# Optimization experiments

Measured on AMD Instinct MI355X. Metric: run time of the kernel, lower is better.

## Reference

```python
import jax, jax.numpy as jnp
import numpy as np


def _mlp2(x, W1, b1, W2, b2):
    # Linear -> (BN=identity in eval) -> ReLU -> Linear  (on_last=False: no act on last)
    return jax.nn.relu(x @ W1 + b1) @ W2 + b2


def _layer(x, ef, row, col, pos, p):
    N, Dn = x.shape
    E, De = ef.shape
    (qW, qB, kW, kB, vW, vB, dW1, dB1, dW2, dB2, eW1, eB1, eW2, eB2,
     attW1, attB1, attW2, attB2, nW1, nB1, nW2, nB2, aW, aB) = p
    d_ep = attW2.shape[0]
    H = De // d_ep
    temp = jnp.sqrt(jnp.asarray(d_ep, x.dtype))
    # ---- reverse-edge lookup: for edge (i,j), find edge (j,i) if present ----
    keys = row.astype(jnp.int64) * N + col.astype(jnp.int64)
    rkeys = col.astype(jnp.int64) * N + row.astype(jnp.int64)
    order = jnp.argsort(keys)
    sk = keys[order]
    loc = jnp.clip(jnp.searchsorted(sk, rkeys), 0, E - 1)
    found = sk[loc] == rkeys
    rev = jnp.where(found[:, None], ef[order[loc]], 0.0)  # [E, De]
    # ---- distance mask ----
    diff = pos[row] - pos[col]                              # [E,3]
    dist = jnp.linalg.norm(diff, axis=1, keepdims=True)     # [E,1]
    dfeat = jnp.concatenate([diff, dist], axis=1)           # [E,4]
    dm = jax.nn.sigmoid(_mlp2(dfeat, dW1, dB1, dW2, dB2))[:, 0]  # [E]
    # ---- message ----
    x_i = x[row]
    x_j = x[col]
    upd_edge = _mlp2(jnp.concatenate([x_i, ef, rev, x_j], axis=1), eW1, eB1, eW2, eB2)  # [E,De]
    q = (x_i @ qW + qB).reshape(E, Dn // H, H)              # [E, d_np, H]
    k = (ef @ kW + kB).reshape(E, d_ep, H)                  # [E, d_ep, H]
    v = x_j @ vW + vB                                       # [E, Da]
    h = jnp.concatenate([q, k], axis=1)                     # [E, d_np+d_ep, H]
    h1 = jax.nn.relu(jnp.einsum('ech,oc->eoh', h, attW1) + attB1[None, :, None])
    att = jnp.einsum('ech,oc->eoh', h1, attW2) + attB2[None, :, None]  # [E, d_ep, H]
    att = att * dm[:, None, None]
    prob = jax.nn.softmax(att / temp, axis=1)               # softmax over channel dim
    wv = prob.reshape(E, -1) * v                            # [E, Da]
    # ---- aggregate (scatter max over source node) ----
    agg = jax.ops.segment_max(wv, row, num_segments=N)
    agg = jnp.where(jnp.isneginf(agg), 0.0, agg)
    # ---- node update ----
    upd_node = _mlp2(jnp.concatenate([x, agg], axis=1), nW1, nB1, nW2, nB2)  # [N,Dn]
    # ---- twin-edge attention (mean of updated edges over out/in edges) ----
    ones = jnp.ones((E,), x.dtype)
    dout = jnp.maximum(jax.ops.segment_sum(ones, row, num_segments=N), 1.0)
    din = jnp.maximum(jax.ops.segment_sum(ones, col, num_segments=N), 1.0)
    outf = jax.ops.segment_sum(upd_edge, row, num_segments=N) / dout[:, None]
    incf = jax.ops.segment_sum(upd_edge, col, num_segments=N) / din[:, None]
    eatt = jax.nn.sigmoid(jnp.concatenate([outf, incf], axis=1) @ aW + aB)  # [N,De]
    final = jax.nn.relu(upd_node) * eatt
    return final, upd_edge, prob


def setup_inputs() -> dict:
    N, E, Dn, De, Da, H, L = 10000, 160000, 128, 128, 128, 8, 2
    d_np, d_ep = Dn // H, De // H
    rng = np.random.default_rng(0)
    half = E // 2
    r = rng.integers(0, N, half)
    c = rng.integers(0, N, half)
    edges = jnp.asarray(np.stack([np.concatenate([r, c]), np.concatenate([c, r])]), dtype=jnp.int32)
    ks = iter(jax.random.split(jax.random.key(0), 40))
    def p(*shape, s=0.02):
        return jax.random.normal(next(ks), shape, jnp.float32) * s
    return dict(
        node_feature=p(N, Dn, s=1.0),
        edge_feature=p(E, De, s=1.0),
        edges_indices=edges,
        descriptor=p(N, 8, s=1.0),
        qW=p(L, Dn, Dn), qB=p(L, Dn),
        kW=p(L, De, De), kB=p(L, De),
        vW=p(L, Dn, Da), vB=p(L, Da),
        dW1=p(L, 4, 32), dB1=p(L, 32),
        dW2=p(L, 32, 1), dB2=p(L, 1),
        eW1=p(L, 2 * Dn + 2 * De, Dn + 2 * De), eB1=p(L, Dn + 2 * De),
        eW2=p(L, Dn + 2 * De, De), eB2=p(L, De),
        attW1=p(L, d_np + d_ep, d_np + d_ep), attB1=p(L, d_np + d_ep),
        attW2=p(L, d_ep, d_np + d_ep), attB2=p(L, d_ep),
        nW1=p(L, Dn + Da, Dn + De), nB1=p(L, Dn + De),
        nW2=p(L, Dn + De, Dn), nB2=p(L, Dn),
        aW=p(L, 2 * De, De), aB=p(L, De),
    )


def reference(node_feature, edge_feature, edges_indices, descriptor,
              qW, qB, kW, kB, vW, vB, dW1, dB1, dW2, dB2,
              eW1, eB1, eW2, eB2, attW1, attB1, attW2, attB2,
              nW1, nB1, nW2, nB2, aW, aB):
    row, col = edges_indices[0], edges_indices[1]
    pos = descriptor[:, :3]
    L = qW.shape[0]
    x, ef = node_feature, edge_feature
    probs = []
    for l in range(L):
        p = (qW[l], qB[l], kW[l], kB[l], vW[l], vB[l], dW1[l], dB1[l], dW2[l], dB2[l],
             eW1[l], eB1[l], eW2[l], eB2[l], attW1[l], attB1[l], attW2[l], attB2[l],
             nW1[l], nB1[l], nW2[l], nB2[l], aW[l], aB[l])
        x, ef, prob = _layer(x, ef, row, col, pos, p)
        if l < L - 1 or L == 1:
            x = jax.nn.relu(x)
            ef = jax.nn.relu(ef)
        probs.append(prob)
    return x, ef, jnp.stack(probs)
```

## Files before the change

kernel.cpp:

```cpp
#include <hip/hip_runtime.h>
#include <math.h>

#define HS 524288
#define HSM (HS - 1)
#define ENC_NEGINF 0x007FFFFFu

__device__ __forceinline__ unsigned encf(float f) {
    unsigned b = __float_as_uint(f);
    return (b & 0x80000000u) ? ~b : (b | 0x80000000u);
}
__device__ __forceinline__ float decf(unsigned u) {
    return __uint_as_float((u & 0x80000000u) ? (u & 0x7FFFFFFFu) : ~u);
}

__device__ __forceinline__ unsigned short f2bf(float x) {
    unsigned u = __float_as_uint(x);
    unsigned r = u + 0x7FFFu + ((u >> 16) & 1u);
    return (unsigned short)(r >> 16);
}
__device__ __forceinline__ float bf2f(unsigned short h) {
    return __uint_as_float(((unsigned)h) << 16);
}

using bfrag = __attribute__((ext_vector_type(8))) short;
using ffrag = __attribute__((ext_vector_type(4))) float;

__device__ __forceinline__ void split8(const float* f, bfrag& hi, bfrag& lo) {
#pragma unroll
    for (int j = 0; j < 8; ++j) {
        unsigned short h = f2bf(f[j]);
        hi[j] = (short)h;
        lo[j] = (short)f2bf(f[j] - bf2f(h));
    }
}


__global__ __launch_bounds__(256) void k_init_static(unsigned* hashK, int* hashV,
                                                     int* rowcnt, int* colcnt, int N) {
    int i = blockIdx.x * 256 + threadIdx.x;
    if (i < HS) { hashK[i] = 0xFFFFFFFFu; hashV[i] = 0x7FFFFFFF; }
    if (i < N) { rowcnt[i] = 0; colcnt[i] = 0; }
}

__global__ __launch_bounds__(256) void k_hash_insert(const int* __restrict__ row,
                                                     const int* __restrict__ col,
                                                     unsigned* hashK, int* hashV, int N, int E) {
    int e = blockIdx.x * 256 + threadIdx.x;
    if (e >= E) return;
    unsigned key = (unsigned)row[e] * (unsigned)N + (unsigned)col[e];
    unsigned h = (key * 2654435761u) >> 13; h &= HSM;
    while (true) {
        unsigned prev = atomicCAS(&hashK[h], 0xFFFFFFFFu, key);
        if (prev == 0xFFFFFFFFu || prev == key) { atomicMin(&hashV[h], e); break; }
        h = (h + 1) & HSM;
    }
}

__global__ __launch_bounds__(256) void k_hash_lookup(const int* __restrict__ row,
                                                     const int* __restrict__ col,
                                                     const unsigned* __restrict__ hashK,
                                                     const int* __restrict__ hashV,
                                                     int* __restrict__ ridx,
                                                     int* rowcnt, int* colcnt, int N, int E) {
    int e = blockIdx.x * 256 + threadIdx.x;
    if (e >= E) return;
    int r = row[e], c = col[e];
    unsigned rkey = (unsigned)c * (unsigned)N + (unsigned)r;
    unsigned h = (rkey * 2654435761u) >> 13; h &= HSM;
    int res = -1;
    while (true) {
        unsigned kk = hashK[h];
        if (kk == rkey) { res = hashV[h]; break; }
        if (kk == 0xFFFFFFFFu) break;
        h = (h + 1) & HSM;
    }
    ridx[e] = res;
    atomicAdd(&rowcnt[r], 1);
    atomicAdd(&colcnt[c], 1);
}

__global__ __launch_bounds__(256) void k_layer_init(unsigned* aggenc, float* outf, float* incf, int NC) {
    int i = blockIdx.x * 256 + threadIdx.x;
    if (i >= NC) return;
    aggenc[i] = ENC_NEGINF;
    outf[i] = 0.f;
    incf[i] = 0.f;
}

__global__ __launch_bounds__(256) void k_prep_wt(const float* __restrict__ src,
                                                 unsigned short* __restrict__ whi,
                                                 unsigned short* __restrict__ wlo,
                                                 int K, int Nn) {
    int idx = blockIdx.x * 256 + threadIdx.x;
    if (idx >= K * Nn) return;
    int k = idx / Nn, n = idx - k * Nn;
    float v = src[idx];
    unsigned short h = f2bf(v);
    float hf = bf2f(h);
    unsigned short l = f2bf(v - hf);
    whi[(size_t)n * K + k] = h;
    wlo[(size_t)n * K + k] = l;
}

template <int ACT>
__global__ __launch_bounds__(256) void k_gemm(const float* __restrict__ A,
                                              const float* __restrict__ B,
                                              const float* __restrict__ bias,
                                              float* __restrict__ C,
                                              int M, int Nd, int K, int lda, int ldb, int ldc) {
    __shared__ float As[16][64];
    __shared__ float Bs[16][64];
    const int tid = threadIdx.x;
    const int bm = blockIdx.y * 64, bn = blockIdx.x * 64;
    const int tx = tid & 15, ty = tid >> 4;
    const int mload = tid >> 2, k4 = (tid & 3) << 2;
    const int kload = tid >> 4, n4 = (tid & 15) << 2;
    float acc[4][4] = {};
    const int gmload = bm + mload;
    const bool avalid = (gmload < M);
    const float* aptr = A + (size_t)(avalid ? gmload : (M - 1)) * lda + k4;
    const float* bptr = B + (size_t)kload * ldb + bn + n4;
    for (int kb = 0; kb < K; kb += 16) {
        float4 av = avalid ? *(const float4*)(aptr + kb) : make_float4(0.f, 0.f, 0.f, 0.f);
        As[k4 + 0][mload] = av.x; As[k4 + 1][mload] = av.y;
        As[k4 + 2][mload] = av.z; As[k4 + 3][mload] = av.w;
        *(float4*)&Bs[kload][n4] = *(const float4*)(bptr + (size_t)kb * ldb);
        __syncthreads();
#pragma unroll
        for (int k = 0; k < 16; ++k) {
            float4 a = *(const float4*)&As[k][ty << 2];
            float4 b = *(const float4*)&Bs[k][tx << 2];
            acc[0][0] += a.x * b.x; acc[0][1] += a.x * b.y; acc[0][2] += a.x * b.z; acc[0][3] += a.x * b.w;
            acc[1][0] += a.y * b.x; acc[1][1] += a.y * b.y; acc[1][2] += a.y * b.z; acc[1][3] += a.y * b.w;
            acc[2][0] += a.z * b.x; acc[2][1] += a.z * b.y; acc[2][2] += a.z * b.z; acc[2][3] += a.z * b.w;
            acc[3][0] += a.w * b.x; acc[3][1] += a.w * b.y; acc[3][2] += a.w * b.z; acc[3][3] += a.w * b.w;
        }
        __syncthreads();
    }
#pragma unroll
    for (int i = 0; i < 4; ++i) {
        int gm = bm + (ty << 2) + i;
        if (gm >= M) continue;
        float* crow = C + (size_t)gm * ldc;
#pragma unroll
        for (int j = 0; j < 4; ++j) {
            int gn = bn + (tx << 2) + j;
            float v = acc[i][j];
            if (bias) v += bias[gn];
            if (ACT == 1) v = fmaxf(v, 0.f);
            if (ACT == 2) v = 1.f / (1.f + __expf(-v));
            crow[gn] = v;
        }
    }
}


#define LDP 40

template <int MODE, int KSTEPS>
__global__ __launch_bounds__(256) void k_mfma_gemm(const float* __restrict__ Asrc,
                                                   const int* __restrict__ ridx,
                                                   const unsigned short* __restrict__ Bhi,
                                                   const unsigned short* __restrict__ Blo,
                                                   const float* __restrict__ bias,
                                                   const float* __restrict__ xa,
                                                   const float* __restrict__ xb,
                                                   const int* __restrict__ rowArr,
                                                   const int* __restrict__ colArr,
                                                   float* __restrict__ outC,
                                                   float* __restrict__ outf,
                                                   float* __restrict__ incf,
                                                   int edgeBase, int Mrows, int reluOut) {
    constexpr int K = KSTEPS * 32;
    __shared__ unsigned short Ah[128 * LDP];
    __shared__ unsigned short Al[128 * LDP];
    __shared__ unsigned short Bh[128 * LDP];
    __shared__ unsigned short Bl[128 * LDP];

    const int tid = threadIdx.x;
    const int bm = blockIdx.y * 128;
    const int bx = blockIdx.x;

    const int sr = tid >> 1;
    const int kh = (tid & 1) * 16;

    const float* p0;
    const float* p1 = nullptr;
    {
        int rc = min(bm + sr, Mrows - 1);
        if (MODE == 0) {
            int e = edgeBase + rc;
            p0 = Asrc + (size_t)e * 128;
            int rv = ridx[e];
            p1 = (rv >= 0) ? (Asrc + (size_t)rv * 128) : nullptr;
        } else if (MODE == 1) {
            p0 = Asrc + (size_t)rc * 384;
        } else {
            p0 = Asrc + (size_t)rc * 128;
        }
    }
    const unsigned short* bhp = Bhi + (size_t)(bx * 128 + sr) * K + kh;
    const unsigned short* blp = Blo + (size_t)(bx * 128 + sr) * K + kh;

    const int wid = tid >> 6;
    const int lane = tid & 63;
    const int wr0 = (wid >> 1) * 64;
    const int wc0 = (wid & 1) * 64;
    const int lm = lane & 15;
    const int lk = (lane >> 4) * 8;

    ffrag acc[4][4];
#pragma unroll
    for (int i = 0; i < 4; ++i)
#pragma unroll
        for (int j = 0; j < 4; ++j)
            acc[i][j] = (ffrag){0.f, 0.f, 0.f, 0.f};

    unsigned short* AhW = &Ah[sr * LDP + kh];
    unsigned short* AlW = &Al[sr * LDP + kh];
    unsigned short* BhW = &Bh[sr * LDP + kh];
    unsigned short* BlW = &Bl[sr * LDP + kh];

    for (int ks = 0; ks < KSTEPS; ++ks) {
        const int kb = ks * 32;
        const float* ap;
        if (MODE == 0) ap = (kb < 128) ? (p0 + kb) : (p1 ? p1 + (kb - 128) : nullptr);
        else ap = p0 + kb;
#pragma unroll
        for (int c = 0; c < 4; ++c) {
            float4 f = ap ? *(const float4*)(ap + kh + c * 4) : make_float4(0.f, 0.f, 0.f, 0.f);
            ushort4 h, l;
            h.x = f2bf(f.x); l.x = f2bf(f.x - bf2f(h.x));
            h.y = f2bf(f.y); l.y = f2bf(f.y - bf2f(h.y));
            h.z = f2bf(f.z); l.z = f2bf(f.z - bf2f(h.z));
            h.w = f2bf(f.w); l.w = f2bf(f.w - bf2f(h.w));
            *(ushort4*)(AhW + c * 4) = h;
            *(ushort4*)(AlW + c * 4) = l;
        }
        {
            uint4 b0 = *(const uint4*)(bhp + kb);
            uint4 b1 = *(const uint4*)(bhp + kb + 8);
            uint4 c0 = *(const uint4*)(blp + kb);
            uint4 c1 = *(const uint4*)(blp + kb + 8);
            *(uint4*)(BhW) = b0; *(uint4*)(BhW + 8) = b1;
            *(uint4*)(BlW) = c0; *(uint4*)(BlW + 8) = c1;
        }
        __syncthreads();
        bfrag a_h[4], a_l[4], b_h[4], b_l[4];
#pragma unroll
        for (int mt = 0; mt < 4; ++mt) {
            int base = (wr0 + mt * 16 + lm) * LDP + lk;
            a_h[mt] = *(const bfrag*)&Ah[base];
            a_l[mt] = *(const bfrag*)&Al[base];
        }
#pragma unroll
        for (int nt = 0; nt < 4; ++nt) {
            int base = (wc0 + nt * 16 + lm) * LDP + lk;
            b_h[nt] = *(const bfrag*)&Bh[base];
            b_l[nt] = *(const bfrag*)&Bl[base];
        }
#pragma unroll
        for (int mt = 0; mt < 4; ++mt)
#pragma unroll
            for (int nt = 0; nt < 4; ++nt) {
                acc[mt][nt] = __builtin_amdgcn_mfma_f32_16x16x32_bf16(a_h[mt], b_h[nt], acc[mt][nt], 0, 0, 0);
                acc[mt][nt] = __builtin_amdgcn_mfma_f32_16x16x32_bf16(a_l[mt], b_h[nt], acc[mt][nt], 0, 0, 0);
                acc[mt][nt] = __builtin_amdgcn_mfma_f32_16x16x32_bf16(a_h[mt], b_l[nt], acc[mt][nt], 0, 0, 0);
            }
        __syncthreads();
    }

    float bv[4];
#pragma unroll
    for (int nt = 0; nt < 4; ++nt) bv[nt] = bias[bx * 128 + wc0 + nt * 16 + lm];

#pragma unroll
    for (int mt = 0; mt < 4; ++mt) {
#pragma unroll
        for (int i = 0; i < 4; ++i) {
            int grow = bm + wr0 + mt * 16 + (lane >> 4) * 4 + i;
            if (grow >= Mrows) continue;
            if (MODE == 0) {
                int e = edgeBase + grow;
                size_t re = (size_t)rowArr[e] * 384;
                size_t ce = (size_t)colArr[e] * 384;
                float* crow = outC + (size_t)grow * 384;
#pragma unroll
                for (int nt = 0; nt < 4; ++nt) {
                    int gcol = bx * 128 + wc0 + nt * 16 + lm;
                    float v = acc[mt][nt][i] + bv[nt] + xa[re + gcol] + xb[ce + gcol];
                    crow[gcol] = fmaxf(v, 0.f);
                }
            } else if (MODE == 1) {
                int e = edgeBase + grow;
                size_t re = (size_t)rowArr[e] * 128;
                size_t ce = (size_t)colArr[e] * 128;
                float* crow = outC + (size_t)e * 128;
#pragma unroll
                for (int nt = 0; nt < 4; ++nt) {
                    int gcol = wc0 + nt * 16 + lm;
                    float v = acc[mt][nt][i] + bv[nt];
                    atomicAdd(&outf[re + gcol], v);
                    atomicAdd(&incf[ce + gcol], v);
                    crow[gcol] = reluOut ? fmaxf(v, 0.f) : v;
                }
            } else {
                float* crow = outC + (size_t)grow * 128;
#pragma unroll
                for (int nt = 0; nt < 4; ++nt) {
                    int gcol = wc0 + nt * 16 + lm;
                    crow[gcol] = acc[mt][nt][i] + bv[nt];
                }
            }
        }
    }
}


__global__ __launch_bounds__(256) void k_dm(const float* __restrict__ desc,
                                            const int* __restrict__ row,
                                            const int* __restrict__ col,
                                            const float* __restrict__ dW1,
                                            const float* __restrict__ dB1,
                                            const float* __restrict__ dW2,
                                            const float* __restrict__ dB2,
                                            float* __restrict__ dmbuf, int E) {
    __shared__ float sw[128];
    __shared__ float sb[32];
    __shared__ float sv[32];
    for (int i = threadIdx.x; i < 128; i += 256) sw[i] = dW1[i];
    if (threadIdx.x < 32) { sb[threadIdx.x] = dB1[threadIdx.x]; sv[threadIdx.x] = dW2[threadIdx.x]; }
    __syncthreads();
    const float db2v = dB2[0];
    for (int e = blockIdx.x * 256 + threadIdx.x; e < E; e += gridDim.x * 256) {
        int r = row[e], c = col[e];
        float dx = desc[r * 8 + 0] - desc[c * 8 + 0];
        float dy = desc[r * 8 + 1] - desc[c * 8 + 1];
        float dz = desc[r * 8 + 2] - desc[c * 8 + 2];
        float dist = sqrtf(dx * dx + dy * dy + dz * dz);
        float acc = db2v;
#pragma unroll
        for (int j = 0; j < 32; ++j) {
            float t = sb[j] + dx * sw[j] + dy * sw[32 + j] + dz * sw[64 + j] + dist * sw[96 + j];
            acc += fmaxf(t, 0.f) * sv[j];
        }
        dmbuf[e] = 1.f / (1.f + __expf(-acc));
    }
}


__global__ __launch_bounds__(256) void k_attn(const float* __restrict__ xq,
                                              const float* __restrict__ kbuf,
                                              const float* __restrict__ xv,
                                              const int* __restrict__ row,
                                              const int* __restrict__ col,
                                              const float* __restrict__ attW1,
                                              const float* __restrict__ attB1,
                                              const float* __restrict__ attW2,
                                              const float* __restrict__ attB2,
                                              const float* __restrict__ dmbuf,
                                              float* __restrict__ prob_out,
                                              unsigned* __restrict__ aggenc, int E) {
    __shared__ float sh1[4][16 * 36];

    const int tid = threadIdx.x;
    const int wv = tid >> 6;
    const int lane = tid & 63;
    const int lm = lane & 15;
    const int lk = lane >> 4;
    float* bounce = sh1[wv];
    const int swz = (lm & 3) << 1;

    bfrag w1h[2], w1l[2], w2h, w2l;
    {
        float tmp[8];
#pragma unroll
        for (int t = 0; t < 2; ++t) {
            const float* p = attW1 + (size_t)(t * 16 + lm) * 32 + lk * 8;
            *(float4*)&tmp[0] = *(const float4*)p;
            *(float4*)&tmp[4] = *(const float4*)(p + 4);
            split8(tmp, w1h[t], w1l[t]);
        }
        const float* p = attW2 + (size_t)lm * 32 + lk * 8;
        *(float4*)&tmp[0] = *(const float4*)p;
        *(float4*)&tmp[4] = *(const float4*)(p + 4);
        split8(tmp, w2h, w2l);
    }
    const float4 b1v0 = *(const float4*)(attB1 + lk * 4);
    const float4 b1v1 = *(const float4*)(attB1 + 16 + lk * 4);
    const float4 b2v = *(const float4*)(attB2 + lk * 4);

    const int gw = (blockIdx.x * 256 + tid) >> 6;
    const int nw = (gridDim.x * 256) >> 6;
    const int ngrp = (E + 1) >> 1;

    for (int g = gw; g < ngrp; g += nw) {
        const int e0 = g * 2;
        const int eL = e0 + (lm >> 3);
        const int ev = min(eL, E - 1);
        const int hd = lm & 7;
        const int rn = row[ev], cn = col[ev];

        float hf[8];
        {
            const float* base = (lk < 2)
                ? (xq + (size_t)rn * 128 + hd + lk * 64)
                : (kbuf + (size_t)ev * 128 + hd + (lk - 2) * 64);
#pragma unroll
            for (int j = 0; j < 8; ++j) hf[j] = base[j * 8];
        }
        bfrag hh, hl;
        split8(hf, hh, hl);

        ffrag d0 = (ffrag){b1v0.x, b1v0.y, b1v0.z, b1v0.w};
        ffrag d1 = (ffrag){b1v1.x, b1v1.y, b1v1.z, b1v1.w};
        d0 = __builtin_amdgcn_mfma_f32_16x16x32_bf16(w1h[0], hh, d0, 0, 0, 0);
        d1 = __builtin_amdgcn_mfma_f32_16x16x32_bf16(w1h[1], hh, d1, 0, 0, 0);
        d0 = __builtin_amdgcn_mfma_f32_16x16x32_bf16(w1l[0], hh, d0, 0, 0, 0);
        d1 = __builtin_amdgcn_mfma_f32_16x16x32_bf16(w1l[1], hh, d1, 0, 0, 0);
        d0 = __builtin_amdgcn_mfma_f32_16x16x32_bf16(w1h[0], hl, d0, 0, 0, 0);
        d1 = __builtin_amdgcn_mfma_f32_16x16x32_bf16(w1h[1], hl, d1, 0, 0, 0);
#pragma unroll
        for (int r = 0; r < 4; ++r) { d0[r] = fmaxf(d0[r], 0.f); d1[r] = fmaxf(d1[r], 0.f); }

        *(float4*)&bounce[lm * 36 + ((lk) ^ swz) * 4] = (float4){d0[0], d0[1], d0[2], d0[3]};
        *(float4*)&bounce[lm * 36 + ((4 + lk) ^ swz) * 4] = (float4){d1[0], d1[1], d1[2], d1[3]};
        __builtin_amdgcn_wave_barrier();
        float h1f[8];
        *(float4*)&h1f[0] = *(const float4*)&bounce[lm * 36 + ((2 * lk) ^ swz) * 4];
        *(float4*)&h1f[4] = *(const float4*)&bounce[lm * 36 + ((2 * lk + 1) ^ swz) * 4];
        __builtin_amdgcn_wave_barrier();
        bfrag h1h, h1l;
        split8(h1f, h1h, h1l);

        ffrag a = (ffrag){b2v.x, b2v.y, b2v.z, b2v.w};
        a = __builtin_amdgcn_mfma_f32_16x16x32_bf16(w2h, h1h, a, 0, 0, 0);
        a = __builtin_amdgcn_mfma_f32_16x16x32_bf16(w2l, h1h, a, 0, 0, 0);
        a = __builtin_amdgcn_mfma_f32_16x16x32_bf16(w2h, h1l, a, 0, 0, 0);

        const float sc = dmbuf[ev] * 0.25f;
        float t0 = a[0] * sc, t1 = a[1] * sc, t2 = a[2] * sc, t3 = a[3] * sc;
        float mx = fmaxf(fmaxf(t0, t1), fmaxf(t2, t3));
        mx = fmaxf(mx, __shfl_xor(mx, 16, 64));
        mx = fmaxf(mx, __shfl_xor(mx, 32, 64));
        float x0 = __expf(t0 - mx), x1 = __expf(t1 - mx);
        float x2 = __expf(t2 - mx), x3 = __expf(t3 - mx);
        float s = x0 + x1 + x2 + x3;
        s += __shfl_xor(s, 16, 64);
        s += __shfl_xor(s, 32, 64);
        const float inv = 1.f / s;
        x0 *= inv; x1 *= inv; x2 *= inv; x3 *= inv;

        if (eL < E) {
            const int ob = lk * 4;
            float* pr = prob_out + (size_t)eL * 128 + hd;
            const float* vp = xv + (size_t)cn * 128 + hd;
            unsigned* ab = aggenc + (size_t)rn * 128 + hd;
            pr[(ob + 0) * 8] = x0;
            pr[(ob + 1) * 8] = x1;
            pr[(ob + 2) * 8] = x2;
            pr[(ob + 3) * 8] = x3;
            atomicMax(&ab[(ob + 0) * 8], encf(x0 * vp[(ob + 0) * 8]));
            atomicMax(&ab[(ob + 1) * 8], encf(x1 * vp[(ob + 1) * 8]));
            atomicMax(&ab[(ob + 2) * 8], encf(x2 * vp[(ob + 2) * 8]));
            atomicMax(&ab[(ob + 3) * 8], encf(x3 * vp[(ob + 3) * 8]));
        }
    }
}


__global__ __launch_bounds__(256) void k_ncat(const float* __restrict__ x,
                                              const unsigned* __restrict__ aggenc,
                                              float* __restrict__ ncat, int N) {
    int i = blockIdx.x * 256 + threadIdx.x;
    if (i >= N * 256) return;
    int n = i >> 8, c = i & 255;
    float v;
    if (c < 128) v = x[n * 128 + c];
    else {
        unsigned u = aggenc[n * 128 + c - 128];
        v = (u == ENC_NEGINF) ? 0.f : decf(u);
    }
    ncat[i] = v;
}

__global__ __launch_bounds__(256) void k_cat2(const float* __restrict__ outf,
                                              const float* __restrict__ incf,
                                              const int* __restrict__ rowcnt,
                                              const int* __restrict__ colcnt,
                                              float* __restrict__ cat2, int N) {
    int i = blockIdx.x * 256 + threadIdx.x;
    if (i >= N * 256) return;
    int n = i >> 8, c = i & 255;
    float v;
    if (c < 128) v = outf[n * 128 + c] / fmaxf((float)rowcnt[n], 1.f);
    else v = incf[n * 128 + c - 128] / fmaxf((float)colcnt[n], 1.f);
    cat2[i] = v;
}

__global__ __launch_bounds__(256) void k_final(const float* __restrict__ un,
                                               const float* __restrict__ eatt,
                                               float* __restrict__ dst, int NC) {
    int i = blockIdx.x * 256 + threadIdx.x;
    if (i >= NC) return;
    dst[i] = fmaxf(un[i], 0.f) * eatt[i];
}


extern "C" void kernel_launch(void* const* d_in, const int* in_sizes, int n_in,
                              void* d_out, int out_size, void* d_ws, size_t ws_size,
                              hipStream_t stream) {
    const float* node_feature = (const float*)d_in[0];
    const float* edge_feature = (const float*)d_in[1];
    const int* edges = (const int*)d_in[2];
    const float* desc = (const float*)d_in[3];
    const float* qW = (const float*)d_in[4];
    const float* qB = (const float*)d_in[5];
    const float* kW = (const float*)d_in[6];
    const float* kB = (const float*)d_in[7];
    const float* vW = (const float*)d_in[8];
    const float* vB = (const float*)d_in[9];
    const float* dW1 = (const float*)d_in[10];
    const float* dB1 = (const float*)d_in[11];
    const float* dW2 = (const float*)d_in[12];
    const float* dB2 = (const float*)d_in[13];
    const float* eW1 = (const float*)d_in[14];
    const float* eB1 = (const float*)d_in[15];
    const float* eW2 = (const float*)d_in[16];
    const float* eB2 = (const float*)d_in[17];
    const float* attW1 = (const float*)d_in[18];
    const float* attB1 = (const float*)d_in[19];
    const float* attW2 = (const float*)d_in[20];
    const float* attB2 = (const float*)d_in[21];
    const float* nW1 = (const float*)d_in[22];
    const float* nB1 = (const float*)d_in[23];
    const float* nW2 = (const float*)d_in[24];
    const float* nB2 = (const float*)d_in[25];
    const float* aW = (const float*)d_in[26];
    const float* aB = (const float*)d_in[27];

    const int N = in_sizes[0] / 128;
    const int E = in_sizes[2] / 2;
    const int L = 2;
    const int* row = edges;
    const int* col = edges + E;

    char* wsp = (char*)d_ws;
    auto alloc = [&](size_t bytes) {
        char* p = wsp;
        wsp += (bytes + 255) & ~(size_t)255;
        return p;
    };
    unsigned* hashK = (unsigned*)alloc((size_t)HS * 4);
    int* hashV = (int*)alloc((size_t)HS * 4);
    int* ridx = (int*)alloc((size_t)E * 4);
    int* rowcnt = (int*)alloc((size_t)N * 4);
    int* colcnt = (int*)alloc((size_t)N * 4);
    float* xq = (float*)alloc((size_t)N * 128 * 4);
    float* xv = (float*)alloc((size_t)N * 128 * 4);
    float* xa = (float*)alloc((size_t)N * 384 * 4);
    float* xb = (float*)alloc((size_t)N * 384 * 4);
    float* kbuf = (float*)alloc((size_t)E * 128 * 4);
    float* efbuf = (float*)alloc((size_t)E * 128 * 4);
    float* dmbuf = (float*)alloc((size_t)E * 4);
    const int CH = 32000;
    float* h1c = (float*)alloc((size_t)CH * 384 * 4);
    unsigned* aggenc = (unsigned*)alloc((size_t)N * 128 * 4);
    float* ncat = (float*)alloc((size_t)N * 256 * 4);
    float* nh1 = (float*)alloc((size_t)N * 256 * 4);
    float* un = (float*)alloc((size_t)N * 128 * 4);
    float* outf = (float*)alloc((size_t)N * 128 * 4);
    float* incf = (float*)alloc((size_t)N * 128 * 4);
    float* cat2 = (float*)alloc((size_t)N * 256 * 4);
    float* eattb = (float*)alloc((size_t)N * 128 * 4);
    float* xbuf = (float*)alloc((size_t)N * 128 * 4);
    unsigned short* wt1_hi = (unsigned short*)alloc((size_t)384 * 256 * 2);
    unsigned short* wt1_lo = (unsigned short*)alloc((size_t)384 * 256 * 2);
    unsigned short* wt2_hi = (unsigned short*)alloc((size_t)128 * 384 * 2);
    unsigned short* wt2_lo = (unsigned short*)alloc((size_t)128 * 384 * 2);
    unsigned short* wtk_hi = (unsigned short*)alloc((size_t)128 * 128 * 2);
    unsigned short* wtk_lo = (unsigned short*)alloc((size_t)128 * 128 * 2);

    float* out_x = (float*)d_out;
    float* out_ef = out_x + (size_t)N * 128;
    float* out_prob = out_ef + (size_t)E * 128;

    k_init_static<<<(HS + 255) / 256, 256, 0, stream>>>(hashK, hashV, rowcnt, colcnt, N);
    k_hash_insert<<<(E + 255) / 256, 256, 0, stream>>>(row, col, hashK, hashV, N, E);
    k_hash_lookup<<<(E + 255) / 256, 256, 0, stream>>>(row, col, hashK, hashV, ridx, rowcnt, colcnt, N, E);

    for (int l = 0; l < L; ++l) {
        const float* x_cur = (l == 0) ? node_feature : xbuf;
        const float* ef_cur = (l == 0) ? edge_feature : efbuf;
        const bool last = (l == L - 1);

        const float* qW_l = qW + (size_t)l * 128 * 128;
        const float* qB_l = qB + (size_t)l * 128;
        const float* kW_l = kW + (size_t)l * 128 * 128;
        const float* kB_l = kB + (size_t)l * 128;
        const float* vW_l = vW + (size_t)l * 128 * 128;
        const float* vB_l = vB + (size_t)l * 128;
        const float* dW1_l = dW1 + (size_t)l * 128;
        const float* dB1_l = dB1 + (size_t)l * 32;
        const float* dW2_l = dW2 + (size_t)l * 32;
        const float* dB2_l = dB2 + (size_t)l * 1;
        const float* eW1_l = eW1 + (size_t)l * 512 * 384;
        const float* eB1_l = eB1 + (size_t)l * 384;
        const float* eW2_l = eW2 + (size_t)l * 384 * 128;
        const float* eB2_l = eB2 + (size_t)l * 128;
        const float* attW1_l = attW1 + (size_t)l * 32 * 32;
        const float* attB1_l = attB1 + (size_t)l * 32;
        const float* attW2_l = attW2 + (size_t)l * 16 * 32;
        const float* attB2_l = attB2 + (size_t)l * 16;
        const float* nW1_l = nW1 + (size_t)l * 256 * 256;
        const float* nB1_l = nB1 + (size_t)l * 256;
        const float* nW2_l = nW2 + (size_t)l * 256 * 128;
        const float* nB2_l = nB2 + (size_t)l * 128;
        const float* aW_l = aW + (size_t)l * 256 * 128;
        const float* aB_l = aB + (size_t)l * 128;

        k_prep_wt<<<(256 * 384 + 255) / 256, 256, 0, stream>>>(eW1_l + (size_t)128 * 384, wt1_hi, wt1_lo, 256, 384);
        k_prep_wt<<<(384 * 128 + 255) / 256, 256, 0, stream>>>(eW2_l, wt2_hi, wt2_lo, 384, 128);
        k_prep_wt<<<(128 * 128 + 255) / 256, 256, 0, stream>>>(kW_l, wtk_hi, wtk_lo, 128, 128);

        k_layer_init<<<(N * 128 + 255) / 256, 256, 0, stream>>>(aggenc, outf, incf, N * 128);

        k_dm<<<(E + 255) / 256, 256, 0, stream>>>(desc, row, col, dW1_l, dB1_l, dW2_l, dB2_l, dmbuf, E);

        int gy_n = (N + 63) / 64;
        k_gemm<0><<<dim3(2, gy_n), 256, 0, stream>>>(x_cur, qW_l, qB_l, xq, N, 128, 128, 128, 128, 128);
        k_gemm<0><<<dim3(2, gy_n), 256, 0, stream>>>(x_cur, vW_l, vB_l, xv, N, 128, 128, 128, 128, 128);
        k_gemm<0><<<dim3(6, gy_n), 256, 0, stream>>>(x_cur, eW1_l, nullptr, xa, N, 384, 128, 128, 384, 384);
        k_gemm<0><<<dim3(6, gy_n), 256, 0, stream>>>(x_cur, eW1_l + (size_t)384 * 384, nullptr, xb, N, 384, 128, 128, 384, 384);
        k_mfma_gemm<2, 4><<<dim3(1, (E + 127) / 128), 256, 0, stream>>>(
            ef_cur, nullptr, wtk_hi, wtk_lo, kB_l, nullptr, nullptr, nullptr, nullptr,
            kbuf, nullptr, nullptr, 0, E, 0);
        k_attn<<<2048, 256, 0, stream>>>(xq, kbuf, xv, row, col, attW1_l, attB1_l, attW2_l, attB2_l,
                                         dmbuf, out_prob + (size_t)l * E * 128, aggenc, E);
        for (int cb = 0; cb < E; cb += CH) {
            int mrows = (E - cb < CH) ? (E - cb) : CH;
            int gy = (mrows + 127) / 128;
            k_mfma_gemm<0, 8><<<dim3(3, gy), 256, 0, stream>>>(
                ef_cur, ridx, wt1_hi, wt1_lo, eB1_l, xa, xb, row, col,
                h1c, nullptr, nullptr, cb, mrows, 0);
            k_mfma_gemm<1, 12><<<dim3(1, gy), 256, 0, stream>>>(
                h1c, nullptr, wt2_hi, wt2_lo, eB2_l, nullptr, nullptr, row, col,
                last ? out_ef : efbuf, outf, incf, cb, mrows, last ? 0 : 1);
        }
        k_ncat<<<(N * 256 + 255) / 256, 256, 0, stream>>>(x_cur, aggenc, ncat, N);
        k_gemm<1><<<dim3(4, gy_n), 256, 0, stream>>>(ncat, nW1_l, nB1_l, nh1, N, 256, 256, 256, 256, 256);
        k_gemm<0><<<dim3(2, gy_n), 256, 0, stream>>>(nh1, nW2_l, nB2_l, un, N, 128, 256, 256, 128, 128);
        k_cat2<<<(N * 256 + 255) / 256, 256, 0, stream>>>(outf, incf, rowcnt, colcnt, cat2, N);
        k_gemm<2><<<dim3(2, gy_n), 256, 0, stream>>>(cat2, aW_l, aB_l, eattb, N, 128, 256, 256, 128, 128);
        k_final<<<(N * 128 + 255) / 256, 256, 0, stream>>>(un, eattb, last ? out_x : xbuf, N * 128);
    }
}
```

Baseline: 2.267 ms.

## Store GEMM activations pre-split into bf16 hi/lo pairs and drop edge chunking

Edge features and the hidden edge-MLP activation are now written as bf16 hi/lo halves by producer kernels and one presplit kernel, so the MFMA GEMMs load ready-made bf16 tiles instead of converting fp32 on every tile load. The hi+lo pair takes the same bytes as the fp32 value it replaces, so global traffic stays roughly the same while per-tile conversion ALU work is removed. The chunk loop over edges is replaced by single full-E launches, which need a full E×384 intermediate buffer. Edge features for the next layer are now kept only in split form, and the final layer writes raw fp32 output.

```diff
diff --git a/kernel.cpp b/kernel.cpp
--- a/kernel.cpp
+++ b/kernel.cpp
@@ -100,6 +100,21 @@
     unsigned short l = f2bf(v - hf);
     whi[(size_t)n * K + k] = h;
     wlo[(size_t)n * K + k] = l;
+}
+
+__global__ __launch_bounds__(256) void k_presplit(const float* __restrict__ src,
+                                                  unsigned short* __restrict__ hi,
+                                                  unsigned short* __restrict__ lo, int n4) {
+    int i = blockIdx.x * 256 + threadIdx.x;
+    if (i >= n4) return;
+    float4 f = ((const float4*)src)[i];
+    ushort4 h, l;
+    h.x = f2bf(f.x); l.x = f2bf(f.x - bf2f(h.x));
+    h.y = f2bf(f.y); l.y = f2bf(f.y - bf2f(h.y));
+    h.z = f2bf(f.z); l.z = f2bf(f.z - bf2f(h.z));
+    h.w = f2bf(f.w); l.w = f2bf(f.w - bf2f(h.w));
+    ((ushort4*)hi)[i] = h;
+    ((ushort4*)lo)[i] = l;
 }
 
 template <int ACT>
@@ -158,7 +173,8 @@
 #define LDP 40
 
 template <int MODE, int KSTEPS>
-__global__ __launch_bounds__(256) void k_mfma_gemm(const float* __restrict__ Asrc,
+__global__ __launch_bounds__(256) void k_mfma_gemm(const unsigned short* __restrict__ Ahi_s,
+                                                   const unsigned short* __restrict__ Alo_s,
                                                    const int* __restrict__ ridx,
                                                    const unsigned short* __restrict__ Bhi,
                                                    const unsigned short* __restrict__ Blo,
@@ -168,10 +184,13 @@
                                                    const int* __restrict__ rowArr,
                                                    const int* __restrict__ colArr,
                                                    float* __restrict__ outC,
+                                                   unsigned short* __restrict__ outHi,
+                                                   unsigned short* __restrict__ outLo,
                                                    float* __restrict__ outf,
                                                    float* __restrict__ incf,
-                                                   int edgeBase, int Mrows, int reluOut) {
+                                                   int Mrows, int rawOut) {
     constexpr int K = KSTEPS * 32;
+    constexpr int AST = (MODE == 1) ? 384 : 128;
     __shared__ unsigned short Ah[128 * LDP];
     __shared__ unsigned short Al[128 * LDP];
     __shared__ unsigned short Bh[128 * LDP];
@@ -184,19 +203,14 @@
     const int sr = tid >> 1;
     const int kh = (tid & 1) * 16;
 
-    const float* p0;
-    const float* p1 = nullptr;
+    const unsigned short *p0h, *p0l, *p1h = nullptr, *p1l = nullptr;
     {
         int rc = min(bm + sr, Mrows - 1);
+        p0h = Ahi_s + (size_t)rc * AST + kh;
+        p0l = Alo_s + (size_t)rc * AST + kh;
         if (MODE == 0) {
-            int e = edgeBase + rc;
-            p0 = Asrc + (size_t)e * 128;
-            int rv = ridx[e];
-            p1 = (rv >= 0) ? (Asrc + (size_t)rv * 128) : nullptr;
-        } else if (MODE == 1) {
-            p0 = Asrc + (size_t)rc * 384;
-        } else {
-            p0 = Asrc + (size_t)rc * 128;
+            int rv = ridx[rc];
+            if (rv >= 0) { p1h = Ahi_s + (size_t)rv * 128 + kh; p1l = Alo_s + (size_t)rv * 128 + kh; }
         }
     }
     const unsigned short* bhp = Bhi + (size_t)(bx * 128 + sr) * K + kh;
@@ -223,19 +237,20 @@
 
     for (int ks = 0; ks < KSTEPS; ++ks) {
         const int kb = ks * 32;
-        const float* ap;
-        if (MODE == 0) ap = (kb < 128) ? (p0 + kb) : (p1 ? p1 + (kb - 128) : nullptr);
-        else ap = p0 + kb;
-#pragma unroll
-        for (int c = 0; c < 4; ++c) {
-            float4 f = ap ? *(const float4*)(ap + kh + c * 4) : make_float4(0.f, 0.f, 0.f, 0.f);
-            ushort4 h, l;
-            h.x = f2bf(f.x); l.x = f2bf(f.x - bf2f(h.x));
-            h.y = f2bf(f.y); l.y = f2bf(f.y - bf2f(h.y));
-            h.z = f2bf(f.z); l.z = f2bf(f.z - bf2f(h.z));
-            h.w = f2bf(f.w); l.w = f2bf(f.w - bf2f(h.w));
-            *(ushort4*)(AhW + c * 4) = h;
-            *(ushort4*)(AlW + c * 4) = l;
+        const unsigned short* sh = p0h + kb;
+        const unsigned short* sl = p0l + kb;
+        if (MODE == 0 && kb >= 128) {
+            sh = p1h ? p1h + (kb - 128) : nullptr;
+            sl = p1l ? p1l + (kb - 128) : nullptr;
+        }
+        {
+            const uint4 z = (uint4){0u, 0u, 0u, 0u};
+            uint4 h0 = sh ? *(const uint4*)(sh) : z;
+            uint4 h1 = sh ? *(const uint4*)(sh + 8) : z;
+            uint4 l0 = sh ? *(const uint4*)(sl) : z;
+            uint4 l1 = sh ? *(const uint4*)(sl + 8) : z;
+            *(uint4*)(AhW) = h0; *(uint4*)(AhW + 8) = h1;
+            *(uint4*)(AlW) = l0; *(uint4*)(AlW + 8) = l1;
         }
         {
             uint4 b0 = *(const uint4*)(bhp + kb);
@@ -281,28 +296,36 @@
             int grow = bm + wr0 + mt * 16 + (lane >> 4) * 4 + i;
             if (grow >= Mrows) continue;
             if (MODE == 0) {
-                int e = edgeBase + grow;
-                size_t re = (size_t)rowArr[e] * 384;
-                size_t ce = (size_t)colArr[e] * 384;
-                float* crow = outC + (size_t)grow * 384;
+                size_t re = (size_t)rowArr[grow] * 384;
+                size_t ce = (size_t)colArr[grow] * 384;
+                unsigned short* hr = outHi + (size_t)grow * 384;
+                unsigned short* lr = outLo + (size_t)grow * 384;
 #pragma unroll
                 for (int nt = 0; nt < 4; ++nt) {
                     int gcol = bx * 128 + wc0 + nt * 16 + lm;
                     float v = acc[mt][nt][i] + bv[nt] + xa[re + gcol] + xb[ce + gcol];
-                    crow[gcol] = fmaxf(v, 0.f);
+                    v = fmaxf(v, 0.f);
+                    unsigned short hb = f2bf(v);
+                    hr[gcol] = hb;
+                    lr[gcol] = f2bf(v - bf2f(hb));
                 }
             } else if (MODE == 1) {
-                int e = edgeBase + grow;
-                size_t re = (size_t)rowArr[e] * 128;
-                size_t ce = (size_t)colArr[e] * 128;
-                float* crow = outC + (size_t)e * 128;
+                size_t re = (size_t)rowArr[grow] * 128;
+                size_t ce = (size_t)colArr[grow] * 128;
 #pragma unroll
                 for (int nt = 0; nt < 4; ++nt) {
                     int gcol = wc0 + nt * 16 + lm;
                     float v = acc[mt][nt][i] + bv[nt];
                     atomicAdd(&outf[re + gcol], v);
                     atomicAdd(&incf[ce + gcol], v);
-                    crow[gcol] = reluOut ? fmaxf(v, 0.f) : v;
+                    if (rawOut) {
+                        outC[(size_t)grow * 128 + gcol] = v;
+                    } else {
+                        float rv = fmaxf(v, 0.f);
+                        unsigned short hb = f2bf(rv);
+                        outHi[(size_t)grow * 128 + gcol] = hb;
+                        outLo[(size_t)grow * 128 + gcol] = f2bf(rv - bf2f(hb));
+                    }
                 }
             } else {
                 float* crow = outC + (size_t)grow * 128;
@@ -561,10 +584,13 @@
     float* xa = (float*)alloc((size_t)N * 384 * 4);
     float* xb = (float*)alloc((size_t)N * 384 * 4);
     float* kbuf = (float*)alloc((size_t)E * 128 * 4);
-    float* efbuf = (float*)alloc((size_t)E * 128 * 4);
     float* dmbuf = (float*)alloc((size_t)E * 4);
-    const int CH = 32000;
-    float* h1c = (float*)alloc((size_t)CH * 384 * 4);
+    unsigned short* efA_hi = (unsigned short*)alloc((size_t)E * 128 * 2);
+    unsigned short* efA_lo = (unsigned short*)alloc((size_t)E * 128 * 2);
+    unsigned short* efB_hi = (unsigned short*)alloc((size_t)E * 128 * 2);
+    unsigned short* efB_lo = (unsigned short*)alloc((size_t)E * 128 * 2);
+    unsigned short* h1hi = (unsigned short*)alloc((size_t)E * 384 * 2);
+    unsigned short* h1lo = (unsigned short*)alloc((size_t)E * 384 * 2);
     unsigned* aggenc = (unsigned*)alloc((size_t)N * 128 * 4);
     float* ncat = (float*)alloc((size_t)N * 256 * 4);
     float* nh1 = (float*)alloc((size_t)N * 256 * 4);
@@ -588,10 +614,14 @@
     k_init_static<<<(HS + 255) / 256, 256, 0, stream>>>(hashK, hashV, rowcnt, colcnt, N);
     k_hash_insert<<<(E + 255) / 256, 256, 0, stream>>>(row, col, hashK, hashV, N, E);
     k_hash_lookup<<<(E + 255) / 256, 256, 0, stream>>>(row, col, hashK, hashV, ridx, rowcnt, colcnt, N, E);
+    k_presplit<<<(E * 32 + 255) / 256, 256, 0, stream>>>(edge_feature, efA_hi, efA_lo, E * 32);
+
+    const int gyE = (E + 127) / 128;
 
     for (int l = 0; l < L; ++l) {
         const float* x_cur = (l == 0) ? node_feature : xbuf;
-        const float* ef_cur = (l == 0) ? edge_feature : efbuf;
+        const unsigned short* efhi = (l == 0) ? efA_hi : efB_hi;
+        const unsigned short* eflo = (l == 0) ? efA_lo : efB_lo;
         const bool last = (l == L - 1);
 
         const float* qW_l = qW + (size_t)l * 128 * 128;
@@ -632,21 +662,17 @@
         k_gemm<0><<<dim3(2, gy_n), 256, 0, stream>>>(x_cur, vW_l, vB_l, xv, N, 128, 128, 128, 128, 128);
         k_gemm<0><<<dim3(6, gy_n), 256, 0, stream>>>(x_cur, eW1_l, nullptr, xa, N, 384, 128, 128, 384, 384);
         k_gemm<0><<<dim3(6, gy_n), 256, 0, stream>>>(x_cur, eW1_l + (size_t)384 * 384, nullptr, xb, N, 384, 128, 128, 384, 384);
-        k_mfma_gemm<2, 4><<<dim3(1, (E + 127) / 128), 256, 0, stream>>>(
-            ef_cur, nullptr, wtk_hi, wtk_lo, kB_l, nullptr, nullptr, nullptr, nullptr,
-            kbuf, nullptr, nullptr, 0, E, 0);
+        k_mfma_gemm<2, 4><<<dim3(1, gyE), 256, 0, stream>>>(
+            efhi, eflo, nullptr, wtk_hi, wtk_lo, kB_l, nullptr, nullptr, nullptr, nullptr,
+            kbuf, nullptr, nullptr, nullptr, nullptr, E, 0);
         k_attn<<<2048, 256, 0, stream>>>(xq, kbuf, xv, row, col, attW1_l, attB1_l, attW2_l, attB2_l,
                                          dmbuf, out_prob + (size_t)l * E * 128, aggenc, E);
-        for (int cb = 0; cb < E; cb += CH) {
-            int mrows = (E - cb < CH) ? (E - cb) : CH;
-            int gy = (mrows + 127) / 128;
-            k_mfma_gemm<0, 8><<<dim3(3, gy), 256, 0, stream>>>(
-                ef_cur, ridx, wt1_hi, wt1_lo, eB1_l, xa, xb, row, col,
-                h1c, nullptr, nullptr, cb, mrows, 0);
-            k_mfma_gemm<1, 12><<<dim3(1, gy), 256, 0, stream>>>(
-                h1c, nullptr, wt2_hi, wt2_lo, eB2_l, nullptr, nullptr, row, col,
-                last ? out_ef : efbuf, outf, incf, cb, mrows, last ? 0 : 1);
-        }
+        k_mfma_gemm<0, 8><<<dim3(3, gyE), 256, 0, stream>>>(
+            efhi, eflo, ridx, wt1_hi, wt1_lo, eB1_l, xa, xb, row, col,
+            nullptr, h1hi, h1lo, nullptr, nullptr, E, 0);
+        k_mfma_gemm<1, 12><<<dim3(1, gyE), 256, 0, stream>>>(
+            h1hi, h1lo, nullptr, wt2_hi, wt2_lo, eB2_l, nullptr, nullptr, row, col,
+            out_ef, efB_hi, efB_lo, outf, incf, E, last ? 1 : 0);
         k_ncat<<<(N * 256 + 255) / 256, 256, 0, stream>>>(x_cur, aggenc, ncat, N);
         k_gemm<1><<<dim3(4, gy_n), 256, 0, stream>>>(ncat, nW1_l, nB1_l, nh1, N, 256, 256, 256, 256, 256);
         k_gemm<0><<<dim3(2, gy_n), 256, 0, stream>>>(nh1, nW2_l, nB2_l, un, N, 128, 256, 256, 128, 128);
```

New measurement: 1.975 ms. 1.15x faster.
